# Performance work log

Measured on AMD Instinct MI355X. Metric: run time of the kernel, lower is better.

## Reference

```python
import jax, jax.numpy as jnp
import numpy as np

B, H, S, D = 65536, 1024, 1024, 128  # batch, hidden_dim, memory_slots, slot_size
WRITE_THRESHOLD = 0.01


def setup_inputs() -> dict:
    key = jax.random.key(0)
    ks = jax.random.split(key, 6)
    return {
        "query": jax.random.normal(ks[0], (B, H), jnp.float32),
        "content": jax.random.normal(ks[1], (B, H), jnp.float32),
        "memory": jax.random.normal(ks[2], (S, D), jnp.float32),
        "memory_age": jnp.zeros((S,), jnp.float32),
        "W_read": jax.random.normal(ks[3], (H, S), jnp.float32) * 0.02,
        "b_read": jnp.zeros((S,), jnp.float32),
        "W_write": jax.random.normal(ks[4], (H, S), jnp.float32) * 0.02,
        "b_write": jnp.zeros((S,), jnp.float32),
        "W_content": jax.random.normal(ks[5], (H, D), jnp.float32) * 0.02,
        "b_content": jnp.zeros((D,), jnp.float32),
    }


def reference(query, content, memory, memory_age, W_read, b_read,
              W_write, b_write, W_content, b_content):
    # ---- read: attention-based addressing over memory slots ----
    read_weights = jax.nn.softmax(query @ W_read + b_read, axis=-1)   # [B, S]
    read_content = read_weights @ memory                              # [B, D]

    # ---- write: vectorized consolidation update (replaces per-slot python loop) ----
    write_weights = jax.nn.softmax(query @ W_write + b_write, axis=-1)  # [B, S]
    w_mean = write_weights.mean(axis=0)                                 # [S]
    c_mean = (content @ W_content + b_content).mean(axis=0)             # [D]
    mask = w_mean > WRITE_THRESHOLD                                     # [S] bool
    consolidation = jax.nn.sigmoid(memory_age * 0.1)                    # [S]
    f = (w_mean * consolidation)[:, None]                               # [S, 1]
    updated = (1.0 - f) * memory + f * c_mean[None, :]                  # [S, D]
    new_memory = jnp.where(mask[:, None], updated, memory)
    new_memory_age = memory_age + mask.astype(memory_age.dtype)

    return read_content, new_memory, new_memory_age
```

## Files before the change

kernel.cpp:

```cpp
#include <hip/hip_runtime.h>
#include <hip/hip_fp16.h>
#include <cstdint>
#include <cstddef>

#define B_N 65536
#define H_N 1024
#define S_N 1024
#define D_N 128

typedef __attribute__((ext_vector_type(8))) short bf16x8;
typedef __attribute__((ext_vector_type(8))) _Float16 f16x8;
typedef __attribute__((ext_vector_type(4))) float f32x4;

#define MFMA_BF(a, b, c) __builtin_amdgcn_mfma_f32_16x16x32_bf16((a), (b), (c), 0, 0, 0)
#define MFMA_F16(a, b, c) __builtin_amdgcn_mfma_f32_16x16x32_f16((a), (b), (c), 0, 0, 0)

__device__ __forceinline__ unsigned short f2bf(float f) {
    unsigned u = __float_as_uint(f);
    u += 0x7FFFu + ((u >> 16) & 1u);
    return (unsigned short)(u >> 16);
}
__device__ __forceinline__ float h2f(unsigned short h) {
    return __half2float(__ushort_as_half(h));
}
__device__ __forceinline__ unsigned short f2h(float f) {
    return __half_as_ushort(__float2half_rn(f));
}
__device__ __forceinline__ void async16(void* lds, const void* g) {
    __builtin_amdgcn_global_load_lds(
        (const __attribute__((address_space(1))) unsigned int*)g,
        (__attribute__((address_space(3))) unsigned int*)lds, 16, 0, 0);
}

__global__ void k_zero(float* p, int n) {
    int i = blockIdx.x * blockDim.x + threadIdx.x;
    if (i < n) p[i] = 0.f;
}

__global__ __launch_bounds__(256) void k_prep_q(const float* __restrict__ q,
                                                unsigned short* __restrict__ qb) {
    size_t i = ((size_t)blockIdx.x * 256 + threadIdx.x) * 8;
    float4 a = *(const float4*)(q + i);
    float4 b = *(const float4*)(q + i + 4);
    uint4 o;
    o.x = (unsigned)f2bf(a.x) | ((unsigned)f2bf(a.y) << 16);
    o.y = (unsigned)f2bf(a.z) | ((unsigned)f2bf(a.w) << 16);
    o.z = (unsigned)f2bf(b.x) | ((unsigned)f2bf(b.y) << 16);
    o.w = (unsigned)f2bf(b.z) | ((unsigned)f2bf(b.w) << 16);
    *(uint4*)(qb + i) = o;
}

__global__ __launch_bounds__(256) void k_prep_w(const float* __restrict__ Wr,
                                                const float* __restrict__ Ww,
                                                unsigned short* __restrict__ wcat) {
    __shared__ float t[32][33];
    const int kb = blockIdx.x * 32, nb = blockIdx.y * 32;
    const float* src = blockIdx.z ? Ww : Wr;
    const int tx = threadIdx.x & 31, ty = threadIdx.x >> 5;
#pragma unroll
    for (int i = 0; i < 4; i++) {
        int r = ty + i * 8;
        t[r][tx] = src[(size_t)(kb + r) * S_N + nb + tx];
    }
    __syncthreads();
    unsigned short* dst = wcat + (size_t)blockIdx.z * 1024 * 1024;
#pragma unroll
    for (int i = 0; i < 4; i++) {
        int r = ty + i * 8;
        dst[(size_t)(nb + r) * 1024 + kb + tx] = f2bf(t[tx][r]);
    }
}

__global__ __launch_bounds__(256) void k_prep_mem(const float* __restrict__ mem,
                                                  unsigned short* __restrict__ memT) {
    __shared__ float t[32][33];
    const int db = blockIdx.x * 32, sb = blockIdx.y * 32;
    const int tx = threadIdx.x & 31, ty = threadIdx.x >> 5;
#pragma unroll
    for (int i = 0; i < 4; i++) {
        int r = ty + i * 8;
        t[r][tx] = mem[(size_t)(sb + r) * D_N + db + tx];
    }
    __syncthreads();
#pragma unroll
    for (int i = 0; i < 4; i++) {
        int r = ty + i * 8;
        memT[(size_t)(db + r) * 1024 + sb + tx] = f2h(t[tx][r]);
    }
}

__global__ __launch_bounds__(256) void k_content(const float* __restrict__ content,
                                                 float* __restrict__ csum) {
    const int tid = threadIdx.x;
    const size_t r0 = (size_t)blockIdx.x * 128;
    float4 a = {0.f, 0.f, 0.f, 0.f};
    const float* base = content + r0 * H_N + tid * 4;
#pragma unroll 8
    for (int r = 0; r < 128; r++) {
        float4 v = *(const float4*)(base + (size_t)r * H_N);
        a.x += v.x; a.y += v.y; a.z += v.z; a.w += v.w;
    }
    atomicAdd(&csum[tid * 4 + 0], a.x);
    atomicAdd(&csum[tid * 4 + 1], a.y);
    atomicAdd(&csum[tid * 4 + 2], a.z);
    atomicAdd(&csum[tid * 4 + 3], a.w);
}

__global__ __launch_bounds__(256) void k_gemm(const unsigned short* __restrict__ qb,
                                              const unsigned short* __restrict__ wcat,
                                              const float* __restrict__ b_read,
                                              const float* __restrict__ b_write,
                                              unsigned short* __restrict__ logits) {
    __shared__ unsigned short aL[4096];
    __shared__ unsigned short bL[4096];
    const int tid = threadIdx.x;
    const int wave = tid >> 6, lane = tid & 63;
    const int wm = wave >> 1, wn = wave & 1;
    const int l16 = lane & 15, g = lane >> 4;
    const int nb = blockIdx.x;
    const size_t mrow = (size_t)blockIdx.y * 128;

    f32x4 acc[4][4];
#pragma unroll
    for (int i = 0; i < 4; i++)
#pragma unroll
        for (int j = 0; j < 4; j++) acc[i][j] = (f32x4){0.f, 0.f, 0.f, 0.f};

    const int a0 = tid >> 2;
    const int s0 = ((tid & 3) ^ ((a0 >> 1) & 3)) * 8;
    const unsigned short* wbase = wcat + (size_t)nb * 128 * 1024;
    const unsigned short* srcA = qb + (mrow + a0) * 1024 + s0;
    const unsigned short* srcB = wbase + (size_t)a0 * 1024 + s0;

    for (int k0 = 0; k0 < 1024; k0 += 32) {
        __syncthreads();
        async16((char*)aL + wave * 1024, srcA + k0);
        async16((char*)aL + 4096 + wave * 1024, srcA + 64 * 1024 + k0);
        async16((char*)bL + wave * 1024, srcB + k0);
        async16((char*)bL + 4096 + wave * 1024, srcB + 64 * 1024 + k0);
        __syncthreads();

        bf16x8 af[4], bv[4];
#pragma unroll
        for (int mt = 0; mt < 4; mt++) {
            int m = wm * 64 + mt * 16 + l16;
            int phys = m * 4 + (g ^ ((m >> 1) & 3));
            af[mt] = *(const bf16x8*)&aL[phys * 8];
        }
#pragma unroll
        for (int nt = 0; nt < 4; nt++) {
            int n = wn * 64 + nt * 16 + l16;
            int phys = n * 4 + (g ^ ((n >> 1) & 3));
            bv[nt] = *(const bf16x8*)&bL[phys * 8];
        }
#pragma unroll
        for (int mt = 0; mt < 4; mt++)
#pragma unroll
            for (int nt = 0; nt < 4; nt++)
                acc[mt][nt] = MFMA_BF(af[mt], bv[nt], acc[mt][nt]);
    }

    const float* bias = (nb < 8) ? b_read : b_write;
    const int cadj = (nb < 8) ? nb * 128 : nb * 128 - 1024;
#pragma unroll
    for (int nt = 0; nt < 4; nt++) {
        const int col = wn * 64 + nt * 16 + l16;
        const float bvv = bias[cadj + col];
#pragma unroll
        for (int mt = 0; mt < 4; mt++) {
            const int row = wm * 64 + mt * 16 + g * 4;
#pragma unroll
            for (int r = 0; r < 4; r++) {
                float e = __expf(acc[mt][nt][r] + bvv);
                logits[(mrow + row + r) * 2048 + nb * 128 + col] = f2h(e);
            }
        }
    }
}

__global__ __launch_bounds__(256) void k_post(const unsigned short* __restrict__ logits,
                                              const unsigned short* __restrict__ memT,
                                              float* __restrict__ out,
                                              float* __restrict__ wpart, int blk0) {
    __shared__ unsigned short L[16 * 2056];
    __shared__ float sInvR[16], sInvW[16];
    const int tid = threadIdx.x;
    const size_t r0 = (size_t)blockIdx.x * 16;
#pragma unroll
    for (int i = 0; i < 16; i++) {
        int c2 = i * 256 + tid;
        int r = c2 >> 8, off = (c2 & 255) * 8;
        *(uint4*)&L[r * 2056 + off] = *(const uint4*)&logits[(r0 + r) * 2048 + off];
    }
    __syncthreads();
    {
        const int r = tid >> 4, sub = tid & 15;
        const unsigned* row = (const unsigned*)&L[r * 2056];
        float zr = 0.f, zw = 0.f;
#pragma unroll 8
        for (int i = 0; i < 32; i++) {
            unsigned u = row[i * 16 + sub];
            zr += h2f((unsigned short)(u & 0xffff)) + h2f((unsigned short)(u >> 16));
            unsigned v = row[512 + i * 16 + sub];
            zw += h2f((unsigned short)(v & 0xffff)) + h2f((unsigned short)(v >> 16));
        }
        zr += __shfl_xor(zr, 1); zr += __shfl_xor(zr, 2);
        zr += __shfl_xor(zr, 4); zr += __shfl_xor(zr, 8);
        zw += __shfl_xor(zw, 1); zw += __shfl_xor(zw, 2);
        zw += __shfl_xor(zw, 4); zw += __shfl_xor(zw, 8);
        if (sub == 0) { sInvR[r] = 1.f / zr; sInvW[r] = 1.f / zw; }
    }
    __syncthreads();
    const int wave = tid >> 6, lane = tid & 63;
    const int l16 = lane & 15, g = lane >> 4;
    f32x4 acc0 = (f32x4){0.f, 0.f, 0.f, 0.f}, acc1 = acc0;
    for (int k0 = 0; k0 < 1024; k0 += 32) {
        f16x8 a  = *(const f16x8*)&L[l16 * 2056 + k0 + g * 8];
        f16x8 b0 = *(const f16x8*)&memT[(size_t)(wave * 32 + l16) * 1024 + k0 + g * 8];
        f16x8 b1 = *(const f16x8*)&memT[(size_t)(wave * 32 + 16 + l16) * 1024 + k0 + g * 8];
        acc0 = MFMA_F16(a, b0, acc0);
        acc1 = MFMA_F16(a, b1, acc1);
    }
#pragma unroll
    for (int r = 0; r < 4; r++) {
        int row = g * 4 + r;
        float iz = sInvR[row];
        out[(r0 + row) * D_N + wave * 32 + l16] = acc0[r] * iz;
        out[(r0 + row) * D_N + wave * 32 + 16 + l16] = acc1[r] * iz;
    }
    float c0 = 0.f, c1 = 0.f, c2 = 0.f, c3 = 0.f;
#pragma unroll
    for (int r = 0; r < 16; r++) {
        float iz = sInvW[r];
        uint2 u = *(const uint2*)&L[r * 2056 + 1024 + tid * 4];
        c0 += h2f((unsigned short)(u.x & 0xffff)) * iz;
        c1 += h2f((unsigned short)(u.x >> 16)) * iz;
        c2 += h2f((unsigned short)(u.y & 0xffff)) * iz;
        c3 += h2f((unsigned short)(u.y >> 16)) * iz;
    }
    float4 o = {c0, c1, c2, c3};
    *(float4*)&wpart[(size_t)(blk0 + blockIdx.x) * 1024 + tid * 4] = o;
}

__global__ __launch_bounds__(256) void k_wreduce(const float* __restrict__ wpart,
                                                 float* __restrict__ wsum) {
    const int c = (blockIdx.x & 3) * 256 + threadIdx.x;
    const int i0 = (blockIdx.x >> 2) * 512;
    float s0 = 0.f, s1 = 0.f;
    for (int i = 0; i < 512; i += 2) {
        s0 += wpart[(size_t)(i0 + i) * 1024 + c];
        s1 += wpart[(size_t)(i0 + i + 1) * 1024 + c];
    }
    atomicAdd(&wsum[c], s0 + s1);
}

__global__ void k_cmean(const float* __restrict__ csum, const float* __restrict__ Wc,
                        const float* __restrict__ bc, float* __restrict__ cmean) {
    const int d = blockIdx.x, t = threadIdx.x;
    float s = 0.f;
#pragma unroll
    for (int j = 0; j < 16; j++) {
        int h = j * 64 + t;
        s += csum[h] * Wc[h * D_N + d];
    }
#pragma unroll
    for (int o = 1; o < 64; o <<= 1) s += __shfl_xor(s, o);
    if (t == 0) cmean[d] = s * (1.0f / (float)B_N) + bc[d];
}

__global__ __launch_bounds__(256) void k_final(const float* __restrict__ memory,
                                               const float* __restrict__ age,
                                               const float* __restrict__ wsum,
                                               const float* __restrict__ cmean,
                                               float* __restrict__ out) {
    const int idx = blockIdx.x * 256 + threadIdx.x;
    const int s = idx >> 7, d = idx & 127;
    const float wm = wsum[s] * (1.0f / (float)B_N);
    const bool mask = wm > 0.01f;
    const float cons = 1.0f / (1.0f + __expf(-0.1f * age[s]));
    const float f = wm * cons;
    const float m = memory[idx];
    const float nm = mask ? ((1.0f - f) * m + f * cmean[d]) : m;
    out[(size_t)B_N * D_N + idx] = nm;
    if (d == 0) out[(size_t)B_N * D_N + (size_t)S_N * D_N + s] = age[s] + (mask ? 1.0f : 0.0f);
}

extern "C" void kernel_launch(void* const* d_in, const int* in_sizes, int n_in,
                              void* d_out, int out_size, void* d_ws, size_t ws_size,
                              hipStream_t stream) {
    const float* query    = (const float*)d_in[0];
    const float* content  = (const float*)d_in[1];
    const float* memory   = (const float*)d_in[2];
    const float* age      = (const float*)d_in[3];
    const float* W_read   = (const float*)d_in[4];
    const float* b_read   = (const float*)d_in[5];
    const float* W_write  = (const float*)d_in[6];
    const float* b_write  = (const float*)d_in[7];
    const float* W_cont   = (const float*)d_in[8];
    const float* b_cont   = (const float*)d_in[9];

    char* ws = (char*)d_ws;
    unsigned short* wcat   = (unsigned short*)ws;
    unsigned short* memT   = (unsigned short*)(ws + (4u << 20));
    float* csum            = (float*)(ws + 4456448);
    float* wsum            = csum + 1024;
    float* cmean           = csum + 2048;
    float* wpart           = (float*)(ws + (8u << 20));
    char* dynbase          = ws + (24u << 20);
    float* out = (float*)d_out;

    long long avail = (long long)ws_size - (24ll << 20);
    long long maxrows = avail > 0 ? avail / 6144 : 0;
    int CB = (int)((maxrows / 128) * 128);
    if (CB > B_N) CB = B_N;
    if (CB < 128) CB = 128;
    unsigned short* qbf    = (unsigned short*)dynbase;
    unsigned short* logits = (unsigned short*)(dynbase + (size_t)CB * 2048);

    k_zero<<<8, 256, 0, stream>>>(csum, 2048);
    k_prep_w<<<dim3(32, 32, 2), 256, 0, stream>>>(W_read, W_write, wcat);
    k_prep_mem<<<dim3(4, 32), 256, 0, stream>>>(memory, memT);
    k_content<<<512, 256, 0, stream>>>(content, csum);

    for (int s0 = 0; s0 < B_N; s0 += CB) {
        int rows = B_N - s0;
        if (rows > CB) rows = CB;
        k_prep_q<<<rows / 2, 256, 0, stream>>>(query + (size_t)s0 * H_N, qbf);
        k_gemm<<<dim3(16, rows / 128), 256, 0, stream>>>(qbf, wcat, b_read, b_write, logits);
        k_post<<<rows / 16, 256, 0, stream>>>(logits, memT, out + (size_t)s0 * D_N,
                                              wpart, s0 / 16);
    }
    k_wreduce<<<32, 256, 0, stream>>>(wpart, wsum);
    k_cmean<<<128, 64, 0, stream>>>(csum, W_cont, b_cont, cmean);
    k_final<<<512, 256, 0, stream>>>(memory, age, wsum, cmean, out);
}
```

Before: 1.178 ms.

## Rewrite logits GEMM with 256x256 tiles, 8 waves, double-buffered LDS pipeline

Replaces the 128x128, 4-wave, single-buffered bf16 GEMM with a 256x256 tile computed by 8 waves. It uses 128KB of double-buffered LDS with a 64-wide K step, interleaves async global-to-LDS loads with MFMA groups under explicit barriers and waitcnts, and raises MFMA priority with setprio. Workgroups are remapped so blocks sharing the same weight tile run close together. The aim is more data reuse per loaded byte and hiding load latency behind compute, at the cost of heavy LDS use, a fragile hand-written schedule, and chunk sizes that must be multiples of 256.

```diff
diff --git a/kernel.cpp b/kernel.cpp
--- a/kernel.cpp
+++ b/kernel.cpp
@@ -106,73 +106,143 @@
     atomicAdd(&csum[tid * 4 + 3], a.w);
 }
 
-__global__ __launch_bounds__(256) void k_gemm(const unsigned short* __restrict__ qb,
-                                              const unsigned short* __restrict__ wcat,
-                                              const float* __restrict__ b_read,
-                                              const float* __restrict__ b_write,
-                                              unsigned short* __restrict__ logits) {
-    __shared__ unsigned short aL[4096];
-    __shared__ unsigned short bL[4096];
+#define BARX() asm volatile("s_barrier" ::: "memory")
+#define LGK0() asm volatile("s_waitcnt lgkmcnt(0)" ::: "memory")
+#define VMC4() asm volatile("s_waitcnt vmcnt(4)" ::: "memory")
+
+__device__ __forceinline__ bf16x8 ldfrag(const char* buf, int row, int ko) {
+    int off = (row * 128 + ko) ^ ((row & 7) << 4);
+    return *(const bf16x8*)(buf + off);
+}
+__device__ __forceinline__ void rd_a(const char* bufA, int wm, int l16, int g, int mh,
+                                     bf16x8 a[4][2]) {
+#pragma unroll
+    for (int m2 = 0; m2 < 4; m2++) {
+        int row = wm * 128 + (mh * 4 + m2) * 16 + l16;
+#pragma unroll
+        for (int ks = 0; ks < 2; ks++) a[m2][ks] = ldfrag(bufA, row, ks * 64 + g * 16);
+    }
+}
+__device__ __forceinline__ void rd_b(const char* bufB, int wn, int l16, int g, int nh,
+                                     bf16x8 b[2][2]) {
+#pragma unroll
+    for (int n2 = 0; n2 < 2; n2++) {
+        int row = wn * 64 + (nh * 2 + n2) * 16 + l16;
+#pragma unroll
+        for (int ks = 0; ks < 2; ks++) b[n2][ks] = ldfrag(bufB, row, ks * 64 + g * 16);
+    }
+}
+__device__ __forceinline__ void mm16(f32x4 acc[8][4], bf16x8 a[4][2], bf16x8 b[2][2],
+                                     int mh, int nh) {
+    __builtin_amdgcn_s_setprio(1);
+#pragma unroll
+    for (int m2 = 0; m2 < 4; m2++)
+#pragma unroll
+        for (int n2 = 0; n2 < 2; n2++) {
+            f32x4 c = acc[mh * 4 + m2][nh * 2 + n2];
+            c = MFMA_BF(a[m2][0], b[n2][0], c);
+            c = MFMA_BF(a[m2][1], b[n2][1], c);
+            acc[mh * 4 + m2][nh * 2 + n2] = c;
+        }
+    __builtin_amdgcn_s_setprio(0);
+}
+
+__global__ __launch_bounds__(512, 2) void k_gemm(const unsigned short* __restrict__ qb,
+                                                 const unsigned short* __restrict__ wcat,
+                                                 const float* __restrict__ b_read,
+                                                 const float* __restrict__ b_write,
+                                                 unsigned short* __restrict__ logits) {
+    __shared__ __align__(16) char sm[131072];
     const int tid = threadIdx.x;
-    const int wave = tid >> 6, lane = tid & 63;
-    const int wm = wave >> 1, wn = wave & 1;
+    const int w = tid >> 6, lane = tid & 63;
+    const int wm = w >> 2, wn = w & 3;
     const int l16 = lane & 15, g = lane >> 4;
-    const int nb = blockIdx.x;
-    const size_t mrow = (size_t)blockIdx.y * 128;
-
-    f32x4 acc[4][4];
-#pragma unroll
-    for (int i = 0; i < 4; i++)
-#pragma unroll
-        for (int j = 0; j < 4; j++) acc[i][j] = (f32x4){0.f, 0.f, 0.f, 0.f};
-
-    const int a0 = tid >> 2;
-    const int s0 = ((tid & 3) ^ ((a0 >> 1) & 3)) * 8;
-    const unsigned short* wbase = wcat + (size_t)nb * 128 * 1024;
-    const unsigned short* srcA = qb + (mrow + a0) * 1024 + s0;
-    const unsigned short* srcB = wbase + (size_t)a0 * 1024 + s0;
-
-    for (int k0 = 0; k0 < 1024; k0 += 32) {
-        __syncthreads();
-        async16((char*)aL + wave * 1024, srcA + k0);
-        async16((char*)aL + 4096 + wave * 1024, srcA + 64 * 1024 + k0);
-        async16((char*)bL + wave * 1024, srcB + k0);
-        async16((char*)bL + 4096 + wave * 1024, srcB + 64 * 1024 + k0);
-        __syncthreads();
-
-        bf16x8 af[4], bv[4];
-#pragma unroll
-        for (int mt = 0; mt < 4; mt++) {
-            int m = wm * 64 + mt * 16 + l16;
-            int phys = m * 4 + (g ^ ((m >> 1) & 3));
-            af[mt] = *(const bf16x8*)&aL[phys * 8];
-        }
-#pragma unroll
-        for (int nt = 0; nt < 4; nt++) {
-            int n = wn * 64 + nt * 16 + l16;
-            int phys = n * 4 + (g ^ ((n >> 1) & 3));
-            bv[nt] = *(const bf16x8*)&bL[phys * 8];
-        }
-#pragma unroll
-        for (int mt = 0; mt < 4; mt++)
-#pragma unroll
-            for (int nt = 0; nt < 4; nt++)
-                acc[mt][nt] = MFMA_BF(af[mt], bv[nt], acc[mt][nt]);
-    }
-
-    const float* bias = (nb < 8) ? b_read : b_write;
-    const int cadj = (nb < 8) ? nb * 128 : nb * 128 - 1024;
+
+    const int nwg = (int)gridDim.y * 8;
+    const int lin = (int)blockIdx.y * 8 + (int)blockIdx.x;
+    const int nlin = (lin & 7) * (nwg >> 3) + (lin >> 3);
+    const int by = nlin >> 3, bx = nlin & 7;
+    const size_t mrow = (size_t)by * 256;
+
+    int g0[2];
+#pragma unroll
+    for (int j = 0; j < 2; j++) {
+        int c = w * 64 + j * 512 + lane;
+        int lc = (c * 16) ^ (((c >> 3) & 7) << 4);
+        g0[j] = (lc >> 7) * 2048 + (lc & 127);
+    }
+    const char* aB = (const char*)qb + mrow * 2048;
+    const char* wB = (const char*)wcat + (size_t)bx * 256 * 2048;
+    char* smW = (char*)sm + w * 1024;
+
+#define STG(d, opb, h, ktB) do {                                              \
+        const char* s_ = ((opb) ? wB : aB) + ((h) * 262144 + (ktB));          \
+        char* d_ = smW + ((d) * 65536 + (opb) * 32768 + (h) * 16384);         \
+        async16(d_,        s_ + g0[0]);                                       \
+        async16(d_ + 8192, s_ + g0[1]);                                       \
+    } while (0)
+
+    f32x4 acc[8][4];
+#pragma unroll
+    for (int m = 0; m < 8; m++)
+#pragma unroll
+        for (int n = 0; n < 4; n++) acc[m][n] = (f32x4){0.f, 0.f, 0.f, 0.f};
+
+    const char* bufA0 = (const char*)sm;
+    const char* bufB0 = (const char*)sm + 32768;
+    const char* bufA1 = (const char*)sm + 65536;
+    const char* bufB1 = (const char*)sm + 98304;
+    bf16x8 a[4][2], b0[2][2], b1[2][2];
+
+    STG(0, 0, 0, 0); STG(0, 1, 0, 0); STG(0, 0, 1, 0); STG(0, 1, 1, 0);
+    STG(1, 1, 0, 128); STG(1, 1, 1, 128);
+    VMC4(); BARX();
+
+#pragma unroll 1
+    for (int i = 0; i < 8; i++) {
+        const int kA = (2 * i + 1) * 128;
+        int t2 = 2 * i + 2; if (t2 > 15) t2 = 15;
+        int t3 = 2 * i + 3; if (t3 > 15) t3 = 15;
+        const int kB = t2 * 128, kC = t3 * 128;
+
+        rd_a(bufA0, wm, l16, g, 0, a); rd_b(bufB0, wn, l16, g, 0, b0);
+        STG(1, 0, 0, kA);
+        BARX(); LGK0(); mm16(acc, a, b0, 0, 0); BARX();
+        rd_b(bufB0, wn, l16, g, 1, b1);
+        STG(1, 0, 1, kA);
+        BARX(); LGK0(); mm16(acc, a, b1, 0, 1); BARX();
+        rd_a(bufA0, wm, l16, g, 1, a);
+        STG(0, 1, 0, kB);
+        BARX(); LGK0(); mm16(acc, a, b1, 1, 1); BARX();
+        STG(0, 1, 1, kB);
+        VMC4(); BARX(); mm16(acc, a, b0, 1, 0); BARX();
+
+        rd_a(bufA1, wm, l16, g, 0, a); rd_b(bufB1, wn, l16, g, 0, b0);
+        STG(0, 0, 0, kB);
+        BARX(); LGK0(); mm16(acc, a, b0, 0, 0); BARX();
+        rd_b(bufB1, wn, l16, g, 1, b1);
+        STG(0, 0, 1, kB);
+        BARX(); LGK0(); mm16(acc, a, b1, 0, 1); BARX();
+        rd_a(bufA1, wm, l16, g, 1, a);
+        STG(1, 1, 0, kC);
+        BARX(); LGK0(); mm16(acc, a, b1, 1, 1); BARX();
+        STG(1, 1, 1, kC);
+        VMC4(); BARX(); mm16(acc, a, b0, 1, 0); BARX();
+    }
+#undef STG
+
+    const float* bias = (bx < 4) ? (b_read + bx * 256) : (b_write + bx * 256 - 1024);
 #pragma unroll
     for (int nt = 0; nt < 4; nt++) {
         const int col = wn * 64 + nt * 16 + l16;
-        const float bvv = bias[cadj + col];
-#pragma unroll
-        for (int mt = 0; mt < 4; mt++) {
-            const int row = wm * 64 + mt * 16 + g * 4;
+        const float bv = bias[col];
+#pragma unroll
+        for (int mt = 0; mt < 8; mt++) {
+            const int row0 = wm * 128 + mt * 16 + g * 4;
 #pragma unroll
             for (int r = 0; r < 4; r++) {
-                float e = __expf(acc[mt][nt][r] + bvv);
-                logits[(mrow + row + r) * 2048 + nb * 128 + col] = f2h(e);
+                float e = __expf(acc[mt][nt][r] + bv);
+                logits[(mrow + row0 + r) * 2048 + (size_t)bx * 256 + col] = f2h(e);
             }
         }
     }
@@ -311,9 +381,9 @@
 
     long long avail = (long long)ws_size - (24ll << 20);
     long long maxrows = avail > 0 ? avail / 6144 : 0;
-    int CB = (int)((maxrows / 128) * 128);
+    int CB = (int)((maxrows / 256) * 256);
     if (CB > B_N) CB = B_N;
-    if (CB < 128) CB = 128;
+    if (CB < 256) CB = 256;
     unsigned short* qbf    = (unsigned short*)dynbase;
     unsigned short* logits = (unsigned short*)(dynbase + (size_t)CB * 2048);
 
@@ -326,7 +396,7 @@
         int rows = B_N - s0;
         if (rows > CB) rows = CB;
         k_prep_q<<<rows / 2, 256, 0, stream>>>(query + (size_t)s0 * H_N, qbf);
-        k_gemm<<<dim3(16, rows / 128), 256, 0, stream>>>(qbf, wcat, b_read, b_write, logits);
+        k_gemm<<<dim3(8, rows / 256), 512, 0, stream>>>(qbf, wcat, b_read, b_write, logits);
         k_post<<<rows / 16, 256, 0, stream>>>(logits, memT, out + (size_t)s0 * D_N,
                                               wpart, s0 / 16);
     }
```

Result: faster. 1.114 ms (-5.4%).
